# Performance work log

Measured on AMD Instinct MI355X. Metric: run time of the kernel, lower is better.

Reference implementation:

```python
import jax, jax.numpy as jnp
import numpy as np

N_NODES = 50000
N_EDGES = 800000


def _norm(deg):
    # DGL: norm = deg^-0.5 with inf (zero-degree) replaced by 0
    return jnp.where(deg > 0, jax.lax.rsqrt(jnp.maximum(deg, 1.0)), 0.0)


def setup_inputs() -> dict:
    key = jax.random.key(0)
    ks = jax.random.split(key, 8)
    x = jax.random.normal(ks[0], (N_NODES, 128), dtype=jnp.float32)
    W1 = jax.random.normal(ks[1], (128, 128), dtype=jnp.float32) * (1.0 / np.sqrt(128))
    b1 = jnp.zeros((128,), dtype=jnp.float32)
    W2 = jax.random.normal(ks[2], (128, 8), dtype=jnp.float32) * (1.0 / np.sqrt(128))
    b2 = jnp.zeros((8,), dtype=jnp.float32)
    src = jax.random.randint(ks[3], (N_EDGES,), 0, N_NODES, dtype=jnp.int32)
    dst = jax.random.randint(ks[4], (N_EDGES,), 0, N_NODES, dtype=jnp.int32)
    graph_ids = jnp.sort(jax.random.randint(ks[5], (N_NODES,), 0, 100, dtype=jnp.int32))
    return {"x": x, "W1": W1, "b1": b1, "W2": W2, "b2": b2,
            "src": src, "dst": dst, "graph_ids": graph_ids, "num_graphs": 100}


def _graph_conv(x, W, b, src, dst, norm_src, norm_dst):
    # GraphConv norm='both': out = D_in^{-1/2} A (D_out^{-1/2} x W) + b
    h = x @ W                                   # [N, F_out]
    msg = h[src] * norm_src[src, None]          # gather + src norm, [E, F_out]
    agg = jax.ops.segment_sum(msg, dst, num_segments=x.shape[0])  # scatter-add
    return agg * norm_dst[:, None] + b


def reference(x, W1, b1, W2, b2, src, dst, graph_ids, num_graphs):
    n = x.shape[0]
    ones_e = jnp.ones((src.shape[0],), dtype=x.dtype)
    deg_out = jax.ops.segment_sum(ones_e, src, num_segments=n)
    deg_in = jax.ops.segment_sum(ones_e, dst, num_segments=n)
    norm_src = _norm(deg_out)
    norm_dst = _norm(deg_in)

    h = _graph_conv(x, W1, b1, src, dst, norm_src, norm_dst)
    h = jax.nn.relu(h)
    h = _graph_conv(h, W2, b2, src, dst, norm_src, norm_dst)

    # dgl.mean_nodes: per-graph mean of node features
    counts = jax.ops.segment_sum(jnp.ones((n,), dtype=x.dtype), graph_ids,
                                 num_segments=num_graphs)
    sums = jax.ops.segment_sum(h, graph_ids, num_segments=num_graphs)
    return sums / jnp.maximum(counts, 1.0)[:, None]
```

## Files before the change

### kernel.cpp

```cpp
#include <hip/hip_runtime.h>

#define F1 128
#define F2 8
#define CAP 64
#define RH 8192
#define ECH 16384

typedef unsigned short us8 __attribute__((ext_vector_type(8)));

__device__ inline unsigned short f2bf(float f) {
  unsigned u = __float_as_uint(f);
  u += 0x7FFF + ((u >> 16) & 1);
  return (unsigned short)(u >> 16);
}
__device__ inline float bf2f(unsigned short h) {
  return __uint_as_float(((unsigned)h) << 16);
}

__global__ void k_pack(const int* __restrict__ src, const int* __restrict__ dst,
                       unsigned short* __restrict__ src16, unsigned short* __restrict__ dst16,
                       int E, int Epad) {
  int e = blockIdx.x * 256 + threadIdx.x;
  if (e < Epad) {
    src16[e] = (e < E) ? (unsigned short)src[e] : (unsigned short)0xFFFF;
    dst16[e] = (e < E) ? (unsigned short)dst[e] : (unsigned short)0xFFFF;
  }
}

__global__ __launch_bounds__(256) void k_hist(const unsigned short* __restrict__ src16,
                                              const unsigned short* __restrict__ dst16,
                                              int* __restrict__ partialA,
                                              int* __restrict__ partialB,
                                              int Epad, int N) {
  __shared__ int binsA[RH];
  __shared__ int binsB[RH];
  int range0 = blockIdx.x * RH;
  int c = blockIdx.y;
  int t = threadIdx.x;
  for (int i = t; i < RH; i += 256) { binsA[i] = 0; binsB[i] = 0; }
  __syncthreads();
  int e0 = c * ECH, e1 = min(e0 + ECH, Epad);
  for (int base = e0 + t * 8; base < e1; base += 2048) {
    us8 a = *(const us8*)&src16[base];
    us8 b = *(const us8*)&dst16[base];
#pragma unroll
    for (int j = 0; j < 8; ++j) {
      int sn = (int)a[j] - range0;
      if ((unsigned)sn < (unsigned)RH) atomicAdd(&binsA[sn], 1);
      int dn = (int)b[j] - range0;
      if ((unsigned)dn < (unsigned)RH) atomicAdd(&binsB[dn], 1);
    }
  }
  __syncthreads();
  for (int i = t; i < RH; i += 256) {
    int n = range0 + i;
    if (n < N) {
      partialA[c * N + n] = binsA[i];
      partialB[c * N + n] = binsB[i];
    }
  }
}

__global__ void k_starts(const int* __restrict__ partialA, const int* __restrict__ partialB,
                         int* __restrict__ starts, int* __restrict__ cnt,
                         float* __restrict__ norm_src, float* __restrict__ norm_dst,
                         int N, int NCH) {
  int n = blockIdx.x * 256 + threadIdx.x;
  if (n < N) {
    int dout = 0;
    for (int c = 0; c < NCH; ++c) dout += partialA[c * N + n];
    int run = n * CAP;
    for (int c = 0; c < NCH; ++c) {
      starts[c * N + n] = run;
      run += partialB[c * N + n];
    }
    int din = run - n * CAP;
    cnt[n] = min(din, CAP);
    norm_src[n] = dout > 0 ? rsqrtf((float)dout) : 0.f;
    norm_dst[n] = din > 0 ? rsqrtf((float)din) : 0.f;
  }
}

__global__ __launch_bounds__(256) void k_scatter(const unsigned short* __restrict__ src16,
                                                 const unsigned short* __restrict__ dst16,
                                                 const int* __restrict__ starts,
                                                 unsigned short* __restrict__ esrc16,
                                                 int Epad, int N) {
  __shared__ int cur[RH];
  int range0 = blockIdx.x * RH;
  int c = blockIdx.y;
  int t = threadIdx.x;
  for (int i = t; i < RH; i += 256) {
    int n = range0 + i;
    cur[i] = (n < N) ? starts[c * N + n] : 0;
  }
  __syncthreads();
  int e0 = c * ECH, e1 = min(e0 + ECH, Epad);
  for (int base = e0 + t * 8; base < e1; base += 2048) {
    us8 a = *(const us8*)&src16[base];
    us8 b = *(const us8*)&dst16[base];
#pragma unroll
    for (int j = 0; j < 8; ++j) {
      int dn = (int)b[j] - range0;
      if ((unsigned)dn < (unsigned)RH) {
        int node = range0 + dn;
        int p = atomicAdd(&cur[dn], 1);
        if (p < (node + 1) * CAP) esrc16[p] = a[j];
      }
    }
  }
}

__global__ __launch_bounds__(256) void k_gemm1(const float* __restrict__ x,
                                               const float* __restrict__ W1,
                                               const float* __restrict__ norm_src,
                                               unsigned short* __restrict__ h1n, int N) {
  __shared__ float Wlds[128 * 64];
  __shared__ float xsT[128 * 64];
  int row0 = blockIdx.x * 64;
  int c0 = blockIdx.y * 64;
  int tid = threadIdx.x;

  for (int i = tid; i < 2048; i += 256) {
    int k = i >> 4;
    int cc = (i & 15) << 2;
    *(float4*)&Wlds[k * 64 + cc] = *(const float4*)&W1[k * 128 + c0 + cc];
  }
  for (int i = tid; i < 2048; i += 256) {
    int r = i & 63;
    int kb = (i >> 6) << 2;
    int grow = row0 + r;
    float4 v = make_float4(0.f, 0.f, 0.f, 0.f);
    if (grow < N) v = *(const float4*)&x[(size_t)grow * 128 + kb];
    xsT[(kb + 0) * 64 + r] = v.x;
    xsT[(kb + 1) * 64 + r] = v.y;
    xsT[(kb + 2) * 64 + r] = v.z;
    xsT[(kb + 3) * 64 + r] = v.w;
  }
  __syncthreads();

  int tc = tid & 15;
  int tr = tid >> 4;
  float acc[4][4] = {{0.f}};
#pragma unroll 4
  for (int k = 0; k < 128; ++k) {
    float4 xv = *(const float4*)&xsT[k * 64 + tr * 4];
    float4 wv = *(const float4*)&Wlds[k * 64 + tc * 4];
    acc[0][0] += xv.x * wv.x; acc[0][1] += xv.x * wv.y; acc[0][2] += xv.x * wv.z; acc[0][3] += xv.x * wv.w;
    acc[1][0] += xv.y * wv.x; acc[1][1] += xv.y * wv.y; acc[1][2] += xv.y * wv.z; acc[1][3] += xv.y * wv.w;
    acc[2][0] += xv.z * wv.x; acc[2][1] += xv.z * wv.y; acc[2][2] += xv.z * wv.z; acc[2][3] += xv.z * wv.w;
    acc[3][0] += xv.w * wv.x; acc[3][1] += xv.w * wv.y; acc[3][2] += xv.w * wv.z; acc[3][3] += xv.w * wv.w;
  }
#pragma unroll
  for (int i = 0; i < 4; ++i) {
    int grow = row0 + tr * 4 + i;
    if (grow < N) {
      float ns = norm_src[grow];
      ushort4 o;
      o.x = f2bf(acc[i][0] * ns);
      o.y = f2bf(acc[i][1] * ns);
      o.z = f2bf(acc[i][2] * ns);
      o.w = f2bf(acc[i][3] * ns);
      *(ushort4*)&h1n[(size_t)grow * 128 + c0 + tc * 4] = o;
    }
  }
}

__global__ __launch_bounds__(256) void k_agg1(const unsigned short* __restrict__ h1n,
                                              const int* __restrict__ cnt,
                                              const unsigned short* __restrict__ esrc16,
                                              const float* __restrict__ norm_dst,
                                              const float* __restrict__ b1,
                                              float* __restrict__ h1b, int N) {
  int wid = (blockIdx.x * 256 + threadIdx.x) >> 6;
  int lane = threadIdx.x & 63;
  if (wid >= N) return;
  int i0 = wid * CAP;
  int i1 = i0 + cnt[wid];
  int q = lane >> 4;
  int fl = lane & 15;
  float acc[8] = {0.f, 0.f, 0.f, 0.f, 0.f, 0.f, 0.f, 0.f};
  for (int i = i0; i < i1; i += 64) {
    int cnt64 = min(64, i1 - i);
    int eid = (i + lane < i1) ? (int)esrc16[i + lane] : -1;
    for (int t = 0; t < cnt64; t += 4) {
      int s = __shfl(eid, t + q);
      if (s >= 0) {
        us8 v = *(const us8*)&h1n[(size_t)s * 128 + fl * 8];
#pragma unroll
        for (int j = 0; j < 8; ++j) acc[j] += bf2f(v[j]);
      }
    }
  }
#pragma unroll
  for (int j = 0; j < 8; ++j) acc[j] += __shfl_down(acc[j], 32);
#pragma unroll
  for (int j = 0; j < 8; ++j) acc[j] += __shfl_down(acc[j], 16);
  if (lane < 16) {
    float nd = norm_dst[wid];
    float4 b0 = *(const float4*)&b1[fl * 8];
    float4 b4 = *(const float4*)&b1[fl * 8 + 4];
    float4 o0, o4;
    o0.x = fmaxf(acc[0] * nd + b0.x, 0.f);
    o0.y = fmaxf(acc[1] * nd + b0.y, 0.f);
    o0.z = fmaxf(acc[2] * nd + b0.z, 0.f);
    o0.w = fmaxf(acc[3] * nd + b0.w, 0.f);
    o4.x = fmaxf(acc[4] * nd + b4.x, 0.f);
    o4.y = fmaxf(acc[5] * nd + b4.y, 0.f);
    o4.z = fmaxf(acc[6] * nd + b4.z, 0.f);
    o4.w = fmaxf(acc[7] * nd + b4.w, 0.f);
    *(float4*)&h1b[(size_t)wid * 128 + fl * 8] = o0;
    *(float4*)&h1b[(size_t)wid * 128 + fl * 8 + 4] = o4;
  }
}

__global__ __launch_bounds__(256) void k_gemm2(const float* __restrict__ h1b,
                                               const float* __restrict__ W2,
                                               const float* __restrict__ norm_src,
                                               float* __restrict__ h2n, int N) {
  __shared__ float W2l[128 * 8];
  int tid = threadIdx.x;
  for (int i = tid; i < 1024; i += 256) W2l[i] = W2[i];
  __syncthreads();
  int g = blockIdx.x * 256 + tid;
  int node = g >> 3, j = g & 7;
  if (node >= N) return;
  const float* row = h1b + (size_t)node * 128;
  float acc = 0.f;
#pragma unroll
  for (int k = 0; k < 128; k += 4) {
    float4 v = *(const float4*)&row[k];
    acc += v.x * W2l[(k + 0) * 8 + j] + v.y * W2l[(k + 1) * 8 + j] +
           v.z * W2l[(k + 2) * 8 + j] + v.w * W2l[(k + 3) * 8 + j];
  }
  h2n[g] = acc * norm_src[node];
}

__global__ __launch_bounds__(256) void k_agg2pool(const float* __restrict__ h2n,
                                                  const int* __restrict__ cnt,
                                                  const unsigned short* __restrict__ esrc16,
                                                  const float* __restrict__ norm_dst,
                                                  const float* __restrict__ b2,
                                                  const int* __restrict__ gids,
                                                  float* __restrict__ gsum, int N) {
  __shared__ float bins[16 * 8];
  __shared__ int sg0;
  int tid = threadIdx.x;
  if (tid < 128) bins[tid] = 0.f;
  int base = blockIdx.x * 32;
  if (tid == 0) sg0 = gids[min(base, N - 1)];
  __syncthreads();
  int node = base + (tid >> 3);
  int j = tid & 7;
  if (node < N) {
    int i0 = node * CAP;
    int i1 = i0 + cnt[node];
    float acc = 0.f;
    for (int i = i0; i < i1; i += 8) {
      int c8 = min(8, i1 - i);
      int eid = (i + j < i1) ? (int)esrc16[i + j] : 0;
      for (int t = 0; t < c8; ++t) {
        int s = __shfl(eid, t, 8);
        acc += h2n[s * 8 + j];
      }
    }
    float r = acc * norm_dst[node] + b2[j];
    int delta = gids[node] - sg0;
    if (delta < 16) atomicAdd(&bins[delta * 8 + j], r);
    else atomicAdd(&gsum[gids[node] * 8 + j], r);
  }
  __syncthreads();
  if (tid < 128) {
    float v = bins[tid];
    if (v != 0.f) atomicAdd(&gsum[(sg0 + (tid >> 3)) * 8 + (tid & 7)], v);
  }
}

__global__ void k_final(const float* __restrict__ gsum, const int* __restrict__ gids,
                        float* __restrict__ out, int NG, int N) {
  int i = blockIdx.x * 256 + threadIdx.x;
  if (i < NG * F2) {
    int g = i >> 3;
    int lo = 0, hi = N;
    while (lo < hi) { int m = (lo + hi) >> 1; if (gids[m] < g) lo = m + 1; else hi = m; }
    int lb = lo;
    lo = 0; hi = N;
    while (lo < hi) { int m = (lo + hi) >> 1; if (gids[m] <= g) lo = m + 1; else hi = m; }
    int cnt = lo - lb;
    out[i] = gsum[i] / fmaxf((float)cnt, 1.f);
  }
}

extern "C" void kernel_launch(void* const* d_in, const int* in_sizes, int n_in,
                              void* d_out, int out_size, void* d_ws, size_t ws_size,
                              hipStream_t stream) {
  const float* x  = (const float*)d_in[0];
  const float* W1 = (const float*)d_in[1];
  const float* b1 = (const float*)d_in[2];
  const float* W2 = (const float*)d_in[3];
  const float* b2 = (const float*)d_in[4];
  const int* src  = (const int*)d_in[5];
  const int* dst  = (const int*)d_in[6];
  const int* gids = (const int*)d_in[7];
  int N = in_sizes[0] / F1;
  int E = in_sizes[5];
  int NG = out_size / F2;
  float* out = (float*)d_out;

  int Epad = (E + 2047) & ~2047;
  int NR  = (N + RH - 1) / RH;
  int NCH = (Epad + ECH - 1) / ECH;

  char* p = (char*)d_ws;
  auto alloc = [&](size_t bytes) -> void* {
    void* r = (void*)p;
    p += (bytes + 255) & ~(size_t)255;
    return r;
  };
  float* gsum    = (float*)alloc((size_t)NG * F2 * 4);
  size_t zero_bytes = (size_t)((char*)p - (char*)gsum);
  unsigned short* src16 = (unsigned short*)alloc((size_t)Epad * 2);
  unsigned short* dst16 = (unsigned short*)alloc((size_t)Epad * 2);
  int* cnt       = (int*)alloc((size_t)N * 4);
  float* norm_src = (float*)alloc((size_t)N * 4);
  float* norm_dst = (float*)alloc((size_t)N * 4);
  unsigned short* esrc16 = (unsigned short*)alloc((size_t)N * CAP * 2);
  unsigned short* h1n = (unsigned short*)alloc((size_t)N * F1 * 2);
  float* h1b     = (float*)alloc((size_t)N * F1 * 4);
  float* h2n     = (float*)alloc((size_t)N * F2 * 4);
  int* partialA  = (int*)h1n;
  int* partialB  = partialA + (size_t)NCH * N;
  int* starts    = partialB + (size_t)NCH * N;
  (void)ws_size; (void)n_in;

  hipMemsetAsync(gsum, 0, zero_bytes, stream);

  k_pack<<<(Epad + 255) / 256, 256, 0, stream>>>(src, dst, src16, dst16, E, Epad);
  k_hist<<<dim3(NR, NCH), 256, 0, stream>>>(src16, dst16, partialA, partialB, Epad, N);
  k_starts<<<(N + 255) / 256, 256, 0, stream>>>(partialA, partialB, starts, cnt,
                                                norm_src, norm_dst, N, NCH);
  k_scatter<<<dim3(NR, NCH), 256, 0, stream>>>(src16, dst16, starts, esrc16, Epad, N);
  k_gemm1<<<dim3((N + 63) / 64, 2), 256, 0, stream>>>(x, W1, norm_src, h1n, N);
  k_agg1<<<(N + 3) / 4, 256, 0, stream>>>(h1n, cnt, esrc16, norm_dst, b1, h1b, N);
  k_gemm2<<<((size_t)N * 8 + 255) / 256, 256, 0, stream>>>(h1b, W2, norm_src, h2n, N);
  k_agg2pool<<<((N * 8 + 255) / 256), 256, 0, stream>>>(h2n, cnt, esrc16, norm_dst, b2, gids, gsum, N);
  k_final<<<(NG * F2 + 255) / 256, 256, 0, stream>>>(gsum, gids, out, NG, N);
}
```

Measured before the change: 249.6 us.

## Fuse second GEMM into layer-1 aggregation and retile first GEMM

Layer-1 aggregation now applies bias, ReLU and the 128x8 W2 projection in registers, with a cross-lane reduction and the src norm. It writes h2n directly, so the fp32 h1b buffer and the separate k_gemm2 pass over it are gone. The first GEMM is retiled to 128-row blocks covering all 128 output columns with K-chunks of 32 and an 8x8 per-thread register tile. That removes the two-column-block split and reloading of x. Partial histogram buffers get their own allocations instead of aliasing h1n, which costs extra workspace. Each wave now also holds 64 floats of W2 in registers, which may lower occupancy.

```diff
diff --git a/kernel.cpp b/kernel.cpp
--- a/kernel.cpp
+++ b/kernel.cpp
@@ -5,6 +5,7 @@
 #define CAP 64
 #define RH 8192
 #define ECH 16384
+#define BK 32
 
 typedef unsigned short us8 __attribute__((ext_vector_type(8)));
 
@@ -115,70 +116,83 @@
                                                const float* __restrict__ W1,
                                                const float* __restrict__ norm_src,
                                                unsigned short* __restrict__ h1n, int N) {
-  __shared__ float Wlds[128 * 64];
-  __shared__ float xsT[128 * 64];
-  int row0 = blockIdx.x * 64;
-  int c0 = blockIdx.y * 64;
+  __shared__ float xsT[BK][132];
+  __shared__ float Wl[BK][132];
+  int row0 = blockIdx.x * 128;
   int tid = threadIdx.x;
-
-  for (int i = tid; i < 2048; i += 256) {
-    int k = i >> 4;
-    int cc = (i & 15) << 2;
-    *(float4*)&Wlds[k * 64 + cc] = *(const float4*)&W1[k * 128 + c0 + cc];
-  }
-  for (int i = tid; i < 2048; i += 256) {
-    int r = i & 63;
-    int kb = (i >> 6) << 2;
-    int grow = row0 + r;
-    float4 v = make_float4(0.f, 0.f, 0.f, 0.f);
-    if (grow < N) v = *(const float4*)&x[(size_t)grow * 128 + kb];
-    xsT[(kb + 0) * 64 + r] = v.x;
-    xsT[(kb + 1) * 64 + r] = v.y;
-    xsT[(kb + 2) * 64 + r] = v.z;
-    xsT[(kb + 3) * 64 + r] = v.w;
-  }
-  __syncthreads();
-
   int tc = tid & 15;
   int tr = tid >> 4;
-  float acc[4][4] = {{0.f}};
-#pragma unroll 4
-  for (int k = 0; k < 128; ++k) {
-    float4 xv = *(const float4*)&xsT[k * 64 + tr * 4];
-    float4 wv = *(const float4*)&Wlds[k * 64 + tc * 4];
-    acc[0][0] += xv.x * wv.x; acc[0][1] += xv.x * wv.y; acc[0][2] += xv.x * wv.z; acc[0][3] += xv.x * wv.w;
-    acc[1][0] += xv.y * wv.x; acc[1][1] += xv.y * wv.y; acc[1][2] += xv.y * wv.z; acc[1][3] += xv.y * wv.w;
-    acc[2][0] += xv.z * wv.x; acc[2][1] += xv.z * wv.y; acc[2][2] += xv.z * wv.z; acc[2][3] += xv.z * wv.w;
-    acc[3][0] += xv.w * wv.x; acc[3][1] += xv.w * wv.y; acc[3][2] += xv.w * wv.z; acc[3][3] += xv.w * wv.w;
-  }
-#pragma unroll
-  for (int i = 0; i < 4; ++i) {
-    int grow = row0 + tr * 4 + i;
+  float acc[8][8] = {{0.f}};
+
+  for (int kb = 0; kb < 128; kb += BK) {
+    __syncthreads();
+#pragma unroll
+    for (int it = 0; it < 4; ++it) {
+      int i = tid + it * 256;
+      int r = i >> 3, kq = i & 7;
+      int grow = row0 + r;
+      float4 v = make_float4(0.f, 0.f, 0.f, 0.f);
+      if (grow < N) v = *(const float4*)&x[(size_t)grow * 128 + kb + kq * 4];
+      xsT[kq * 4 + 0][r] = v.x;
+      xsT[kq * 4 + 1][r] = v.y;
+      xsT[kq * 4 + 2][r] = v.z;
+      xsT[kq * 4 + 3][r] = v.w;
+    }
+#pragma unroll
+    for (int it = 0; it < 4; ++it) {
+      int i = tid + it * 256;
+      int k = i >> 5, c4 = i & 31;
+      *(float4*)&Wl[k][c4 * 4] = *(const float4*)&W1[(size_t)(kb + k) * 128 + c4 * 4];
+    }
+    __syncthreads();
+#pragma unroll 2
+    for (int k = 0; k < BK; ++k) {
+      float4 xa = *(float4*)&xsT[k][tr * 8];
+      float4 xb = *(float4*)&xsT[k][tr * 8 + 4];
+      float4 wa = *(float4*)&Wl[k][tc * 8];
+      float4 wb = *(float4*)&Wl[k][tc * 8 + 4];
+      float xs[8] = {xa.x, xa.y, xa.z, xa.w, xb.x, xb.y, xb.z, xb.w};
+      float ws[8] = {wa.x, wa.y, wa.z, wa.w, wb.x, wb.y, wb.z, wb.w};
+#pragma unroll
+      for (int i = 0; i < 8; ++i)
+#pragma unroll
+        for (int j = 0; j < 8; ++j) acc[i][j] += xs[i] * ws[j];
+    }
+  }
+#pragma unroll
+  for (int i = 0; i < 8; ++i) {
+    int grow = row0 + tr * 8 + i;
     if (grow < N) {
       float ns = norm_src[grow];
-      ushort4 o;
-      o.x = f2bf(acc[i][0] * ns);
-      o.y = f2bf(acc[i][1] * ns);
-      o.z = f2bf(acc[i][2] * ns);
-      o.w = f2bf(acc[i][3] * ns);
-      *(ushort4*)&h1n[(size_t)grow * 128 + c0 + tc * 4] = o;
-    }
-  }
-}
-
-__global__ __launch_bounds__(256) void k_agg1(const unsigned short* __restrict__ h1n,
-                                              const int* __restrict__ cnt,
-                                              const unsigned short* __restrict__ esrc16,
-                                              const float* __restrict__ norm_dst,
-                                              const float* __restrict__ b1,
-                                              float* __restrict__ h1b, int N) {
+      us8 o;
+#pragma unroll
+      for (int j = 0; j < 8; ++j) o[j] = f2bf(acc[i][j] * ns);
+      *(us8*)&h1n[(size_t)grow * 128 + tc * 8] = o;
+    }
+  }
+}
+
+__global__ __launch_bounds__(256) void k_agg1f(const unsigned short* __restrict__ h1n,
+                                               const int* __restrict__ cnt,
+                                               const unsigned short* __restrict__ esrc16,
+                                               const float* __restrict__ norm_dst,
+                                               const float* __restrict__ norm_src,
+                                               const float* __restrict__ b1,
+                                               const float* __restrict__ W2,
+                                               float* __restrict__ h2n, int N) {
   int wid = (blockIdx.x * 256 + threadIdx.x) >> 6;
   int lane = threadIdx.x & 63;
+  int q = lane >> 4;
+  int fl = lane & 15;
+  float4 w2a[8], w2b[8];
+#pragma unroll
+  for (int jj = 0; jj < 8; ++jj) {
+    w2a[jj] = *(const float4*)&W2[(fl * 8 + jj) * 8];
+    w2b[jj] = *(const float4*)&W2[(fl * 8 + jj) * 8 + 4];
+  }
   if (wid >= N) return;
   int i0 = wid * CAP;
   int i1 = i0 + cnt[wid];
-  int q = lane >> 4;
-  int fl = lane & 15;
   float acc[8] = {0.f, 0.f, 0.f, 0.f, 0.f, 0.f, 0.f, 0.f};
   for (int i = i0; i < i1; i += 64) {
     int cnt64 = min(64, i1 - i);
@@ -196,44 +210,41 @@
   for (int j = 0; j < 8; ++j) acc[j] += __shfl_down(acc[j], 32);
 #pragma unroll
   for (int j = 0; j < 8; ++j) acc[j] += __shfl_down(acc[j], 16);
-  if (lane < 16) {
-    float nd = norm_dst[wid];
-    float4 b0 = *(const float4*)&b1[fl * 8];
-    float4 b4 = *(const float4*)&b1[fl * 8 + 4];
-    float4 o0, o4;
-    o0.x = fmaxf(acc[0] * nd + b0.x, 0.f);
-    o0.y = fmaxf(acc[1] * nd + b0.y, 0.f);
-    o0.z = fmaxf(acc[2] * nd + b0.z, 0.f);
-    o0.w = fmaxf(acc[3] * nd + b0.w, 0.f);
-    o4.x = fmaxf(acc[4] * nd + b4.x, 0.f);
-    o4.y = fmaxf(acc[5] * nd + b4.y, 0.f);
-    o4.z = fmaxf(acc[6] * nd + b4.z, 0.f);
-    o4.w = fmaxf(acc[7] * nd + b4.w, 0.f);
-    *(float4*)&h1b[(size_t)wid * 128 + fl * 8] = o0;
-    *(float4*)&h1b[(size_t)wid * 128 + fl * 8 + 4] = o4;
-  }
-}
-
-__global__ __launch_bounds__(256) void k_gemm2(const float* __restrict__ h1b,
-                                               const float* __restrict__ W2,
-                                               const float* __restrict__ norm_src,
-                                               float* __restrict__ h2n, int N) {
-  __shared__ float W2l[128 * 8];
-  int tid = threadIdx.x;
-  for (int i = tid; i < 1024; i += 256) W2l[i] = W2[i];
-  __syncthreads();
-  int g = blockIdx.x * 256 + tid;
-  int node = g >> 3, j = g & 7;
-  if (node >= N) return;
-  const float* row = h1b + (size_t)node * 128;
-  float acc = 0.f;
-#pragma unroll
-  for (int k = 0; k < 128; k += 4) {
-    float4 v = *(const float4*)&row[k];
-    acc += v.x * W2l[(k + 0) * 8 + j] + v.y * W2l[(k + 1) * 8 + j] +
-           v.z * W2l[(k + 2) * 8 + j] + v.w * W2l[(k + 3) * 8 + j];
-  }
-  h2n[g] = acc * norm_src[node];
+  float nd = norm_dst[wid];
+  float4 bb0 = *(const float4*)&b1[fl * 8];
+  float4 bb1 = *(const float4*)&b1[fl * 8 + 4];
+  float r[8];
+  r[0] = fmaxf(acc[0] * nd + bb0.x, 0.f);
+  r[1] = fmaxf(acc[1] * nd + bb0.y, 0.f);
+  r[2] = fmaxf(acc[2] * nd + bb0.z, 0.f);
+  r[3] = fmaxf(acc[3] * nd + bb0.w, 0.f);
+  r[4] = fmaxf(acc[4] * nd + bb1.x, 0.f);
+  r[5] = fmaxf(acc[5] * nd + bb1.y, 0.f);
+  r[6] = fmaxf(acc[6] * nd + bb1.z, 0.f);
+  r[7] = fmaxf(acc[7] * nd + bb1.w, 0.f);
+  float4 pa = make_float4(0.f, 0.f, 0.f, 0.f);
+  float4 pb = make_float4(0.f, 0.f, 0.f, 0.f);
+#pragma unroll
+  for (int jj = 0; jj < 8; ++jj) {
+    pa.x += r[jj] * w2a[jj].x; pa.y += r[jj] * w2a[jj].y;
+    pa.z += r[jj] * w2a[jj].z; pa.w += r[jj] * w2a[jj].w;
+    pb.x += r[jj] * w2b[jj].x; pb.y += r[jj] * w2b[jj].y;
+    pb.z += r[jj] * w2b[jj].z; pb.w += r[jj] * w2b[jj].w;
+  }
+#pragma unroll
+  for (int d = 8; d >= 1; d >>= 1) {
+    pa.x += __shfl_down(pa.x, d); pa.y += __shfl_down(pa.y, d);
+    pa.z += __shfl_down(pa.z, d); pa.w += __shfl_down(pa.w, d);
+    pb.x += __shfl_down(pb.x, d); pb.y += __shfl_down(pb.y, d);
+    pb.z += __shfl_down(pb.z, d); pb.w += __shfl_down(pb.w, d);
+  }
+  if (lane == 0) {
+    float ns = norm_src[wid];
+    pa.x *= ns; pa.y *= ns; pa.z *= ns; pa.w *= ns;
+    pb.x *= ns; pb.y *= ns; pb.z *= ns; pb.w *= ns;
+    *(float4*)&h2n[(size_t)wid * 8] = pa;
+    *(float4*)&h2n[(size_t)wid * 8 + 4] = pb;
+  }
 }
 
 __global__ __launch_bounds__(256) void k_agg2pool(const float* __restrict__ h2n,
@@ -326,11 +337,10 @@
   float* norm_dst = (float*)alloc((size_t)N * 4);
   unsigned short* esrc16 = (unsigned short*)alloc((size_t)N * CAP * 2);
   unsigned short* h1n = (unsigned short*)alloc((size_t)N * F1 * 2);
-  float* h1b     = (float*)alloc((size_t)N * F1 * 4);
   float* h2n     = (float*)alloc((size_t)N * F2 * 4);
-  int* partialA  = (int*)h1n;
-  int* partialB  = partialA + (size_t)NCH * N;
-  int* starts    = partialB + (size_t)NCH * N;
+  int* partialA  = (int*)alloc((size_t)NCH * N * 4);
+  int* partialB  = (int*)alloc((size_t)NCH * N * 4);
+  int* starts    = (int*)alloc((size_t)NCH * N * 4);
   (void)ws_size; (void)n_in;
 
   hipMemsetAsync(gsum, 0, zero_bytes, stream);
@@ -340,9 +350,8 @@
   k_starts<<<(N + 255) / 256, 256, 0, stream>>>(partialA, partialB, starts, cnt,
                                                 norm_src, norm_dst, N, NCH);
   k_scatter<<<dim3(NR, NCH), 256, 0, stream>>>(src16, dst16, starts, esrc16, Epad, N);
-  k_gemm1<<<dim3((N + 63) / 64, 2), 256, 0, stream>>>(x, W1, norm_src, h1n, N);
-  k_agg1<<<(N + 3) / 4, 256, 0, stream>>>(h1n, cnt, esrc16, norm_dst, b1, h1b, N);
-  k_gemm2<<<((size_t)N * 8 + 255) / 256, 256, 0, stream>>>(h1b, W2, norm_src, h2n, N);
+  k_gemm1<<<(N + 127) / 128, 256, 0, stream>>>(x, W1, norm_src, h1n, N);
+  k_agg1f<<<(N + 3) / 4, 256, 0, stream>>>(h1n, cnt, esrc16, norm_dst, norm_src, b1, W2, h2n, N);
   k_agg2pool<<<((N * 8 + 255) / 256), 256, 0, stream>>>(h2n, cnt, esrc16, norm_dst, b2, gids, gsum, N);
   k_final<<<(NG * F2 + 255) / 256, 256, 0, stream>>>(gsum, gids, out, NG, N);
 }
```

Measured after the change: 317.8 us. 27.3% more time.
